# Kernel tuning notes

Hardware: AMD Instinct MI355X
Metric: run time of the kernel (lower is better)

The kernel has to match this reference:

```python
import jax, jax.numpy as jnp
import numpy as np

DEPTH = 6
HEADS = 8
DIM = 512
DH = DIM // HEADS          # 64
SEQ = 512
BATCH = 8
MEM = 4096                 # KNN memory slots per batch element (scaled from 64000)
TOPK = 32                  # num_retrieved_memories
KNN_LAYERS = (3, 4)        # memorizing_layers=(4,5), 1-indexed -> 0-indexed 3,4
FF = 4 * DIM


def setup_inputs() -> dict:
    key = jax.random.key(0)
    ks = jax.random.split(key, 18)
    s = 0.02
    return {
        "x":     jax.random.normal(ks[0], (BATCH, SEQ, DIM), jnp.float32),
        "Wq":    jax.random.normal(ks[1], (DEPTH, DIM, DIM), jnp.float32) * s,
        "Wk":    jax.random.normal(ks[2], (DEPTH, DIM, DIM), jnp.float32) * s,
        "Wv":    jax.random.normal(ks[3], (DEPTH, DIM, DIM), jnp.float32) * s,
        "Wo":    jax.random.normal(ks[4], (DEPTH, DIM, DIM), jnp.float32) * s,
        "ln1_s": jnp.ones((DEPTH, DIM), jnp.float32),
        "ln1_b": jnp.zeros((DEPTH, DIM), jnp.float32),
        "ln2_s": jnp.ones((DEPTH, DIM), jnp.float32),
        "ln2_b": jnp.zeros((DEPTH, DIM), jnp.float32),
        "W1":    jax.random.normal(ks[5], (DEPTH, DIM, FF), jnp.float32) * s,
        "W2":    jax.random.normal(ks[6], (DEPTH, FF, DIM), jnp.float32) * s,
        "lnf_s": jnp.ones((DIM,), jnp.float32),
        "lnf_b": jnp.zeros((DIM,), jnp.float32),
        # pre-populated KNN memory banks (keys/values in head dim), one per memorizing layer
        "mem_k": jax.random.normal(ks[7], (len(KNN_LAYERS), BATCH, MEM, DH), jnp.float32),
        "mem_v": jax.random.normal(ks[8], (len(KNN_LAYERS), BATCH, MEM, DH), jnp.float32),
    }


def _ln(x, s, b):
    m = x.mean(-1, keepdims=True)
    v = ((x - m) ** 2).mean(-1, keepdims=True)
    return (x - m) * jax.lax.rsqrt(v + 1e-5) * s + b


def _gather_mem(mem, idx):
    # mem: (b, M, d), idx: (b, h, n, K) -> (b, h, n, K, d)
    return jax.vmap(lambda m, i: m[i])(mem, idx)


def reference(x, Wq, Wk, Wv, Wo, ln1_s, ln1_b, ln2_s, ln2_b, W1, W2,
              lnf_s, lnf_b, mem_k, mem_v):
    b, n, d = x.shape
    scale = DH ** -0.5
    causal = jnp.tril(jnp.ones((n, n), dtype=bool))
    neg = jnp.float32(-1e9)
    mem_i = 0
    for l in range(DEPTH):
        h = _ln(x, ln1_s[l], ln1_b[l])
        q = (h @ Wq[l]).reshape(b, n, HEADS, DH)
        k = (h @ Wk[l]).reshape(b, n, HEADS, DH)
        v = (h @ Wv[l]).reshape(b, n, HEADS, DH)
        sim = jnp.einsum('bihd,bjhd->bhij', q, k) * scale
        sim = jnp.where(causal, sim, neg)
        if l in KNN_LAYERS:
            mk, mv = mem_k[mem_i], mem_v[mem_i]              # (b, M, dh)
            # KNN search: dense scoring + top-k retrieval
            sim_all = jnp.einsum('bihd,bmd->bhim', q, mk) * scale  # (b,h,n,M)
            top_sim, top_idx = jax.lax.top_k(sim_all, TOPK)        # (b,h,n,K)
            gv = _gather_mem(mv, top_idx)                          # (b,h,n,K,dh)
            # joint softmax over [retrieved memories, local causal]
            logits = jnp.concatenate([top_sim, sim], axis=-1)
            attn = jax.nn.softmax(logits, axis=-1)
            a_mem, a_loc = attn[..., :TOPK], attn[..., TOPK:]
            out = (jnp.einsum('bhik,bhikd->bhid', a_mem, gv)
                   + jnp.einsum('bhij,bjhd->bhid', a_loc, v))
            mem_i += 1
        else:
            attn = jax.nn.softmax(sim, axis=-1)
            out = jnp.einsum('bhij,bjhd->bhid', attn, v)
        out = out.transpose(0, 2, 1, 3).reshape(b, n, d) @ Wo[l]
        x = x + out
        h2 = _ln(x, ln2_s[l], ln2_b[l])
        x = x + jax.nn.gelu(h2 @ W1[l]) @ W2[l]
    return _ln(x, lnf_s, lnf_b)
```

## Files before the change

kernel.cpp:

```cpp
#include <hip/hip_runtime.h>
#include <math.h>

#define BB 8
#define NN 512
#define DD 512
#define HH 8
#define DHH 64
#define FFF 2048
#define MEMM 4096
#define TOPKK 32
#define DEPTHH 6
#define NT (BB*NN)

typedef __bf16 bf16x8 __attribute__((ext_vector_type(8)));
typedef __bf16 bf16x4 __attribute__((ext_vector_type(4)));
typedef float f32x4 __attribute__((ext_vector_type(4)));

template <int OBF16>
__global__ __launch_bounds__(256) void ln_kernel(const float* __restrict__ xin,
                                                 const float* __restrict__ g,
                                                 const float* __restrict__ bt,
                                                 void* __restrict__ outv) {
  __shared__ float red[4];
  int tok = blockIdx.x;
  const float* xr = xin + (size_t)tok * DD;
  int t = threadIdx.x;
  float v0 = xr[t], v1 = xr[t + 256];
  float s = v0 + v1;
#pragma unroll
  for (int m = 32; m; m >>= 1) s += __shfl_xor(s, m, 64);
  if ((t & 63) == 0) red[t >> 6] = s;
  __syncthreads();
  float mean = (red[0] + red[1] + red[2] + red[3]) * (1.0f / 512.0f);
  float d0 = v0 - mean, d1 = v1 - mean;
  float vv = d0 * d0 + d1 * d1;
#pragma unroll
  for (int m = 32; m; m >>= 1) vv += __shfl_xor(vv, m, 64);
  __syncthreads();
  if ((t & 63) == 0) red[t >> 6] = vv;
  __syncthreads();
  float var = (red[0] + red[1] + red[2] + red[3]) * (1.0f / 512.0f);
  float inv = rsqrtf(var + 1e-5f);
  float o0 = d0 * inv * g[t] + bt[t];
  float o1 = d1 * inv * g[t + 256] + bt[t + 256];
  if (OBF16) {
    __bf16* out = (__bf16*)outv;
    out[(size_t)tok * DD + t] = (__bf16)o0;
    out[(size_t)tok * DD + t + 256] = (__bf16)o1;
  } else {
    float* out = (float*)outv;
    out[(size_t)tok * DD + t] = o0;
    out[(size_t)tok * DD + t + 256] = o1;
  }
}

__device__ inline float gelu_f(float x) {
  float x3 = x * x * x;
  return 0.5f * x * (1.0f + tanhf(0.7978845608028654f * (x + 0.044715f * x3)));
}

__global__ __launch_bounds__(256) void transpose_bf16_kernel(const float* __restrict__ src,
                                                             __bf16* __restrict__ dst,
                                                             int K, int N) {
  __shared__ float tile[32][33];
  int n0 = blockIdx.x * 32, k0 = blockIdx.y * 32;
  int tx = threadIdx.x & 31, ty = threadIdx.x >> 5;
#pragma unroll
  for (int i = 0; i < 4; i++) {
    int r = ty + i * 8;
    tile[r][tx] = src[(size_t)(k0 + r) * N + n0 + tx];
  }
  __syncthreads();
#pragma unroll
  for (int i = 0; i < 4; i++) {
    int r = ty + i * 8;
    dst[(size_t)(n0 + r) * K + k0 + tx] = (__bf16)tile[tx][r];
  }
}

template <int EPI, int OBF16>
__global__ __launch_bounds__(256) void gemm_mfma(const __bf16* __restrict__ A,
                                                 const __bf16* __restrict__ Bt,
                                                 const float* __restrict__ R,
                                                 void* __restrict__ Cout,
                                                 int M, int N, int K) {
  __shared__ __bf16 Als[128 * 72];
  __shared__ __bf16 Bls[64 * 72];
  int t = threadIdx.x;
  int bn = blockIdx.x, bm = blockIdx.y;
  int lane = t & 63, wave = t >> 6;
  int wr = wave >> 1, wc = wave & 1;
  int m15 = lane & 15, q = lane >> 4;
  f32x4 acc[4][2] = {};
  for (int kt = 0; kt < K; kt += 64) {
    __syncthreads();
#pragma unroll
    for (int i = 0; i < 4; i++) {
      int c = t + i * 256;
      int row = c >> 3, pb = c & 7;
      *(uint4*)&Als[row * 72 + pb * 8] =
          *(const uint4*)(A + (size_t)(bm * 128 + row) * K + kt + pb * 8);
    }
#pragma unroll
    for (int i = 0; i < 2; i++) {
      int c = t + i * 256;
      int row = c >> 3, pb = c & 7;
      *(uint4*)&Bls[row * 72 + pb * 8] =
          *(const uint4*)(Bt + (size_t)(bn * 64 + row) * K + kt + pb * 8);
    }
    __syncthreads();
#pragma unroll
    for (int ks = 0; ks < 2; ks++) {
      bf16x8 af[4], bf[2];
#pragma unroll
      for (int mt = 0; mt < 4; mt++)
        af[mt] = *(const bf16x8*)&Als[(wr * 64 + mt * 16 + m15) * 72 + (ks * 4 + q) * 8];
#pragma unroll
      for (int nt = 0; nt < 2; nt++)
        bf[nt] = *(const bf16x8*)&Bls[(wc * 32 + nt * 16 + m15) * 72 + (ks * 4 + q) * 8];
#pragma unroll
      for (int mt = 0; mt < 4; mt++)
#pragma unroll
        for (int nt = 0; nt < 2; nt++)
          acc[mt][nt] = __builtin_amdgcn_mfma_f32_16x16x32_bf16(af[mt], bf[nt],
                                                                acc[mt][nt], 0, 0, 0);
    }
  }
#pragma unroll
  for (int mt = 0; mt < 4; mt++) {
#pragma unroll
    for (int nt = 0; nt < 2; nt++) {
      int gc = bn * 64 + wc * 32 + nt * 16 + m15;
#pragma unroll
      for (int r = 0; r < 4; r++) {
        int gr = bm * 128 + wr * 64 + mt * 16 + q * 4 + r;
        size_t off = (size_t)gr * N + gc;
        float v = acc[mt][nt][r];
        if (EPI == 1) v = gelu_f(v);
        if (EPI == 2) v += R[off];
        if (OBF16) ((__bf16*)Cout)[off] = (__bf16)v;
        else       ((float*)Cout)[off] = v;
      }
    }
  }
}

__global__ __launch_bounds__(256) void split_bf16_kernel(const float* __restrict__ src,
                                                         __bf16* __restrict__ hi,
                                                         __bf16* __restrict__ lo) {
  int i = blockIdx.x * 256 + threadIdx.x;
  float4 v = ((const float4*)src)[i];
  float xs[4] = {v.x, v.y, v.z, v.w};
  bf16x4 hv, lv;
#pragma unroll
  for (int e = 0; e < 4; e++) {
    __bf16 h = (__bf16)xs[e];
    hv[e] = h;
    lv[e] = (__bf16)(xs[e] - (float)h);
  }
  *(bf16x4*)&hi[(size_t)i * 4] = hv;
  *(bf16x4*)&lo[(size_t)i * 4] = lv;
}

__global__ __launch_bounds__(256) void vtrans_split_kernel(const float* __restrict__ v,
                                                           __bf16* __restrict__ vth,
                                                           __bf16* __restrict__ vtl) {
  __shared__ float tile[64 * 68];
  int tt = blockIdx.x, h = blockIdx.y, b = blockIdx.z;
  int t = threadIdx.x;
#pragma unroll
  for (int i = 0; i < 4; i++) {
    int lin = i * 256 + t, row = lin >> 4, c = (lin & 15) * 4;
    float4 x = *(const float4*)(v + ((size_t)(b * NN) + tt * 64 + row) * DD + h * DHH + c);
    *(float4*)&tile[row * 68 + c] = x;
  }
  __syncthreads();
  int d = t >> 2, tb = (t & 3) * 16;
  float xs[16];
#pragma unroll
  for (int j = 0; j < 16; j++) xs[j] = tile[(tb + j) * 68 + d];
  bf16x8 h0, h1, l0, l1;
#pragma unroll
  for (int j = 0; j < 8; j++) {
    __bf16 a = (__bf16)xs[j];
    h0[j] = a; l0[j] = (__bf16)(xs[j] - (float)a);
    __bf16 bmv = (__bf16)xs[8 + j];
    h1[j] = bmv; l1[j] = (__bf16)(xs[8 + j] - (float)bmv);
  }
  size_t ob = ((size_t)(b * HH + h) * 64 + d) * NN + tt * 64 + tb;
  *(bf16x8*)(vth + ob) = h0; *(bf16x8*)(vth + ob + 8) = h1;
  *(bf16x8*)(vtl + ob) = l0; *(bf16x8*)(vtl + ob + 8) = l1;
}

__global__ __launch_bounds__(256) void knn_score_mfma(const float* __restrict__ q,
                                                      const __bf16* __restrict__ khi,
                                                      const __bf16* __restrict__ klo,
                                                      float* __restrict__ S,
                                                      int bh0) {
  __shared__ __bf16 Kls[2][128 * 72];
  int it = blockIdx.x, bh = bh0 + blockIdx.y;
  int b = bh >> 3, h = bh & 7;
  int t = threadIdx.x;
  int lane = t & 63, w = t >> 6;
  int m15 = lane & 15, kg = lane >> 4;
  const float scale = 0.125f;

  bf16x8 aqh[2][2], aql[2][2];
#pragma unroll
  for (int rf = 0; rf < 2; rf++)
#pragma unroll
    for (int ks = 0; ks < 2; ks++) {
      const float* qp = q + ((size_t)(b * NN) + it * 32 + rf * 16 + m15) * DD +
                        h * DHH + ks * 32 + kg * 8;
      float4 x0 = *(const float4*)qp;
      float4 x1 = *(const float4*)(qp + 4);
      float xs[8] = {x0.x, x0.y, x0.z, x0.w, x1.x, x1.y, x1.z, x1.w};
#pragma unroll
      for (int e = 0; e < 8; e++) {
        __bf16 hv = (__bf16)xs[e];
        aqh[rf][ks][e] = hv;
        aql[rf][ks][e] = (__bf16)(xs[e] - (float)hv);
      }
    }

  const __bf16* khb = khi + (size_t)b * MEMM * DHH;
  const __bf16* klb = klo + (size_t)b * MEMM * DHH;
  size_t srow0 = (size_t)blockIdx.y * NN + it * 32;

  for (int mt = 0; mt < MEMM; mt += 128) {
    __syncthreads();
#pragma unroll
    for (int i = 0; i < 4; i++) {
      int lin = i * 256 + t;
      int row = lin >> 3, cb = (lin & 7) * 8;
      *(uint4*)&Kls[0][row * 72 + cb] = *(const uint4*)(khb + (size_t)(mt + row) * DHH + cb);
      *(uint4*)&Kls[1][row * 72 + cb] = *(const uint4*)(klb + (size_t)(mt + row) * DHH + cb);
    }
    __syncthreads();
    f32x4 acc[2][2] = {};
#pragma unroll
    for (int ks = 0; ks < 2; ks++) {
      bf16x8 bh2[2], bl2[2];
#pragma unroll
      for (int cf = 0; cf < 2; cf++) {
        int row = w * 32 + cf * 16 + m15;
        bh2[cf] = *(const bf16x8*)&Kls[0][row * 72 + ks * 32 + kg * 8];
        bl2[cf] = *(const bf16x8*)&Kls[1][row * 72 + ks * 32 + kg * 8];
      }
#pragma unroll
      for (int rf = 0; rf < 2; rf++)
#pragma unroll
        for (int cf = 0; cf < 2; cf++) {
          acc[rf][cf] = __builtin_amdgcn_mfma_f32_16x16x32_bf16(aqh[rf][ks], bh2[cf], acc[rf][cf], 0, 0, 0);
          acc[rf][cf] = __builtin_amdgcn_mfma_f32_16x16x32_bf16(aql[rf][ks], bh2[cf], acc[rf][cf], 0, 0, 0);
          acc[rf][cf] = __builtin_amdgcn_mfma_f32_16x16x32_bf16(aqh[rf][ks], bl2[cf], acc[rf][cf], 0, 0, 0);
        }
    }
#pragma unroll
    for (int rf = 0; rf < 2; rf++)
#pragma unroll
      for (int cf = 0; cf < 2; cf++) {
        int col = mt + w * 32 + cf * 16 + m15;
#pragma unroll
        for (int rr = 0; rr < 4; rr++)
          S[(srow0 + rf * 16 + kg * 4 + rr) * MEMM + col] = acc[rf][cf][rr] * scale;
      }
  }
}

__global__ __launch_bounds__(256, 4) void knn_select_kernel(const float* __restrict__ S,
                                                            float* __restrict__ topv,
                                                            int* __restrict__ topi,
                                                            int row_base) {
  int lane = threadIdx.x & 63;
  int row = blockIdx.x * 4 + (threadIdx.x >> 6);
  const float* srow = S + (size_t)row * MEMM;
  unsigned u[64];
#pragma unroll
  for (int i = 0; i < 64; i++) {
    union { float f; unsigned b; } cv;
    cv.f = srow[i * 64 + lane];
    unsigned b = cv.b;
    u[i] = (b & 0x80000000u) ? ~b : (b | 0x80000000u);
  }
  unsigned T = 0;
#pragma unroll 1
  for (int bit = 31; bit >= 0; --bit) {
    unsigned Tp = T | (1u << bit);
    int c = 0;
#pragma unroll
    for (int i = 0; i < 64; i++) c += (u[i] >= Tp) ? 1 : 0;
#pragma unroll
    for (int m = 32; m; m >>= 1) c += __shfl_xor(c, m, 64);
    if (c >= TOPKK) {
      T = Tp;
      if (c == TOPKK) break;
    }
  }
  unsigned long long below = (1ull << lane) - 1ull;
  float* tvrow = topv + (size_t)(row_base + row) * TOPKK;
  int* tirow = topi + (size_t)(row_base + row) * TOPKK;
  int g = 0;
#pragma unroll
  for (int i = 0; i < 64; i++) {
    bool f = u[i] > T;
    unsigned long long m = __ballot(f);
    if (f) {
      int pos = g + __popcll(m & below);
      union { unsigned b; float f2; } rv;
      rv.b = (u[i] & 0x80000000u) ? (u[i] & 0x7fffffffu) : ~u[i];
      tvrow[pos] = rv.f2;
      tirow[pos] = i * 64 + lane;
    }
    g += __popcll(m);
  }
#pragma unroll
  for (int i = 0; i < 64; i++) {
    if (g < TOPKK) {
      bool f = (u[i] == T);
      unsigned long long m = __ballot(f);
      if (f) {
        int pos = g + __popcll(m & below);
        if (pos < TOPKK) {
          union { unsigned b; float f2; } rv;
          rv.b = (T & 0x80000000u) ? (T & 0x7fffffffu) : ~T;
          tvrow[pos] = rv.f2;
          tirow[pos] = i * 64 + lane;
        }
      }
      g += __popcll(m);
    }
  }
}

__device__ __forceinline__ void insert32vi(float (&rtv)[32], int (&rti)[32],
                                           float sv, int idx, float& thr) {
  float mv = rtv[0], mv2 = INFINITY;
  int mi = 0;
#pragma unroll
  for (int k = 1; k < 32; k++) {
    float v = rtv[k];
    bool lt = v < mv;
    mv2 = lt ? mv : fminf(mv2, v);
    mv = lt ? v : mv;
    mi = lt ? k : mi;
  }
#pragma unroll
  for (int k = 0; k < 32; k++) {
    bool hit = (k == mi);
    rtv[k] = hit ? sv : rtv[k];
    rti[k] = hit ? idx : rti[k];
  }
  thr = fminf(mv2, sv);
}

__global__ __launch_bounds__(256) void knn_mfma_topk(const float* __restrict__ q,
                                                     const __bf16* __restrict__ khi,
                                                     const __bf16* __restrict__ klo,
                                                     float* __restrict__ topv,
                                                     int* __restrict__ topi) {
  __shared__ __bf16 Kls[2][128 * 72];
  __shared__ float scb[32][132];
  __shared__ unsigned short midx[32 * 260];
  __shared__ float rthr[8][32];
  int it = blockIdx.x, h = blockIdx.y, b = blockIdx.z;
  int t = threadIdx.x;
  int lane = t & 63, w = t >> 6;
  int m15 = lane & 15, kg = lane >> 4;
  const float scale = 0.125f;
  bf16x8 aqh[2][2], aql[2][2];
#pragma unroll
  for (int rf = 0; rf < 2; rf++)
#pragma unroll
    for (int ks = 0; ks < 2; ks++) {
      const float* qp = q + ((size_t)(b * NN) + it * 32 + rf * 16 + m15) * DD +
                        h * DHH + ks * 32 + kg * 8;
      float4 x0 = *(const float4*)qp;
      float4 x1 = *(const float4*)(qp + 4);
      float xs[8] = {x0.x, x0.y, x0.z, x0.w, x1.x, x1.y, x1.z, x1.w};
#pragma unroll
      for (int e = 0; e < 8; e++) {
        __bf16 hv = (__bf16)xs[e];
        aqh[rf][ks][e] = hv;
        aql[rf][ks][e] = (__bf16)(xs[e] - (float)hv);
      }
    }
  int r = t & 31, p = t >> 5;
  rthr[p][r] = -INFINITY;
  float rtv[32]; int rti[32];
#pragma unroll
  for (int k = 0; k < 32; k++) { rtv[k] = -INFINITY; rti[k] = 0; }
  float thr = -INFINITY;
  const __bf16* khb = khi + (size_t)b * MEMM * DHH;
  const __bf16* klb = klo + (size_t)b * MEMM * DHH;

  for (int mt = 0; mt < MEMM; mt += 128) {
    __syncthreads();
#pragma unroll
    for (int i = 0; i < 4; i++) {
      int lin = i * 256 + t;
      int row = lin >> 3, cb = (lin & 7) * 8;
      *(uint4*)&Kls[0][row * 72 + cb] = *(const uint4*)(khb + (size_t)(mt + row) * DHH + cb);
      *(uint4*)&Kls[1][row * 72 + cb] = *(const uint4*)(klb + (size_t)(mt + row) * DHH + cb);
    }
    __syncthreads();
    f32x4 acc[2][2] = {};
#pragma unroll
    for (int ks = 0; ks < 2; ks++) {
      bf16x8 bh2[2], bl2[2];
#pragma unroll
      for (int cf = 0; cf < 2; cf++) {
        int row = w * 32 + cf * 16 + m15;
        bh2[cf] = *(const bf16x8*)&Kls[0][row * 72 + ks * 32 + kg * 8];
        bl2[cf] = *(const bf16x8*)&Kls[1][row * 72 + ks * 32 + kg * 8];
      }
#pragma unroll
      for (int rf = 0; rf < 2; rf++)
#pragma unroll
        for (int cf = 0; cf < 2; cf++) {
          acc[rf][cf] = __builtin_amdgcn_mfma_f32_16x16x32_bf16(aqh[rf][ks], bh2[cf], acc[rf][cf], 0, 0, 0);
          acc[rf][cf] = __builtin_amdgcn_mfma_f32_16x16x32_bf16(aql[rf][ks], bh2[cf], acc[rf][cf], 0, 0, 0);
          acc[rf][cf] = __builtin_amdgcn_mfma_f32_16x16x32_bf16(aqh[rf][ks], bl2[cf], acc[rf][cf], 0, 0, 0);
        }
    }
#pragma unroll
    for (int rf = 0; rf < 2; rf++)
#pragma unroll
      for (int cf = 0; cf < 2; cf++) {
        int col = w * 32 + cf * 16 + m15;
#pragma unroll
        for (int rr = 0; rr < 4; rr++)
          scb[rf * 16 + kg * 4 + rr][col] = acc[rf][cf][rr] * scale;
      }
    __syncthreads();
    {
      float B2 = rthr[0][r];
#pragma unroll
      for (int j = 1; j < 8; j++) B2 = fmaxf(B2, rthr[j][r]);
      const float* srow = &scb[r][16 * p];
#pragma unroll 1
      for (int c = 0; c < 16; c++) {
        int cc = (c + r) & 15;
        float sv = srow[cc];
        if (sv > fmaxf(thr, B2))
          insert32vi(rtv, rti, sv, mt + 16 * p + cc, thr);
      }
      rthr[p][r] = thr;
    }
  }
  __syncthreads();
  float* mvals = (float*)&Kls[0][0];
#pragma unroll
  for (int k = 0; k < 32; k++) {
    int cc = (k + r) & 31;
    mvals[(size_t)260 * r + 32 * p + cc] = rtv[k];
    midx[(size_t)260 * r + 32 * p + cc] = (unsigned short)rti[k];
  }
  __syncthreads();
  if (t < 32) {
#pragma unroll 1
    for (int c = 0; c < 224; c++) {
      int cc = c + r; if (cc >= 224) cc -= 224;
      float sv = mvals[(size_t)260 * r + 32 + cc];
      if (sv > thr)
        insert32vi(rtv, rti, sv, (int)midx[(size_t)260 * r + 32 + cc], thr);
    }
    size_t rowg = ((size_t)b * HH + h) * NN + it * 32 + r;
#pragma unroll
    for (int k = 0; k < 32; k++) {
      topv[rowg * TOPKK + k] = rtv[k];
      topi[rowg * TOPKK + k] = rti[k];
    }
  }
}

__global__ __launch_bounds__(256) void attn_mfma_kernel(
    const float* __restrict__ q, const float* __restrict__ kf,
    const __bf16* __restrict__ vth, const __bf16* __restrict__ vtl,
    __bf16* __restrict__ ao, const float* __restrict__ topv,
    const int* __restrict__ topi, const float* __restrict__ mem_v, int knn) {
  __shared__ __align__(16) __bf16 smem[27648];
  __bf16* Kh = smem;
  __bf16* Kl = smem + 4608;
  __bf16* Vh = smem + 9216;
  __bf16* Vl = smem + 13824;
  __bf16* Pw = smem + 18432;

  int bi = blockIdx.x, h = blockIdx.y, b = blockIdx.z;
  int t = threadIdx.x, lane = t & 63, w = t >> 6;
  int q15 = lane & 15, g = lane >> 4;
  const float scale = 0.125f;

  bf16x8 qh[2], ql[2];
  {
    const float* qp = q + ((size_t)(b * NN) + bi * 64 + w * 16 + q15) * DD + h * DHH;
#pragma unroll
    for (int ks = 0; ks < 2; ks++) {
      float4 x0 = *(const float4*)(qp + ks * 32 + g * 8);
      float4 x1 = *(const float4*)(qp + ks * 32 + g * 8 + 4);
      float xs[8] = {x0.x, x0.y, x0.z, x0.w, x1.x, x1.y, x1.z, x1.w};
#pragma unroll
      for (int e = 0; e < 8; e++) {
        __bf16 hv = (__bf16)xs[e];
        qh[ks][e] = hv;
        ql[ks][e] = (__bf16)(xs[e] - (float)hv);
      }
    }
  }
  float m_run = -INFINITY, l_run = 0.f;
  f32x4 opv[4] = {};
  int ntiles = bi + 1;
  for (int jt = 0; jt < ntiles; jt++) {
    __syncthreads();
#pragma unroll
    for (int i = 0; i < 4; i++) {
      int lin = i * 256 + t, row = lin >> 4, c = (lin & 15) * 4;
      float4 kx = *(const float4*)(kf + ((size_t)(b * NN) + jt * 64 + row) * DD + h * DHH + c);
      float ks4[4] = {kx.x, kx.y, kx.z, kx.w};
      bf16x4 hv, lv;
#pragma unroll
      for (int e = 0; e < 4; e++) {
        __bf16 a = (__bf16)ks4[e];
        hv[e] = a; lv[e] = (__bf16)(ks4[e] - (float)a);
      }
      *(bf16x4*)&Kh[row * 72 + c] = hv;
      *(bf16x4*)&Kl[row * 72 + c] = lv;
    }
#pragma unroll
    for (int i = 0; i < 2; i++) {
      int lin = i * 256 + t, d = lin >> 3, tb = (lin & 7) * 8;
      size_t go = ((size_t)(b * HH + h) * 64 + d) * NN + jt * 64 + tb;
      *(uint4*)&Vh[d * 72 + tb] = *(const uint4*)(vth + go);
      *(uint4*)&Vl[d * 72 + tb] = *(const uint4*)(vtl + go);
    }
    __syncthreads();
    int smax = (jt == bi) ? w : 3;
    float sc16[16];
    float tmax = -INFINITY;
#pragma unroll
    for (int s = 0; s < 4; s++) {
      if (s <= smax) {
        f32x4 accs = {};
#pragma unroll
        for (int ks = 0; ks < 2; ks++) {
          bf16x8 ah = *(const bf16x8*)&Kh[(s * 16 + q15) * 72 + ks * 32 + g * 8];
          bf16x8 al = *(const bf16x8*)&Kl[(s * 16 + q15) * 72 + ks * 32 + g * 8];
          accs = __builtin_amdgcn_mfma_f32_16x16x32_bf16(ah, qh[ks], accs, 0, 0, 0);
          accs = __builtin_amdgcn_mfma_f32_16x16x32_bf16(al, qh[ks], accs, 0, 0, 0);
          accs = __builtin_amdgcn_mfma_f32_16x16x32_bf16(ah, ql[ks], accs, 0, 0, 0);
        }
#pragma unroll
        for (int r = 0; r < 4; r++) {
          float sv = accs[r] * scale;
          if (jt == bi) {
            int kvg = jt * 64 + s * 16 + g * 4 + r;
            int qg = bi * 64 + w * 16 + q15;
            if (kvg > qg) sv = -INFINITY;
          }
          sc16[s * 4 + r] = sv;
          tmax = fmaxf(tmax, sv);
        }
      } else {
#pragma unroll
        for (int r = 0; r < 4; r++) sc16[s * 4 + r] = -INFINITY;
      }
    }
    tmax = fmaxf(tmax, __shfl_xor(tmax, 16, 64));
    tmax = fmaxf(tmax, __shfl_xor(tmax, 32, 64));
    float m_new = fmaxf(m_run, tmax);
    float psum = 0.f;
    __bf16 ph[16], pl[16];
#pragma unroll
    for (int i = 0; i < 16; i++) {
      float p = __expf(sc16[i] - m_new);
      psum += p;
      __bf16 hp = (__bf16)p;
      ph[i] = hp; pl[i] = (__bf16)(p - (float)hp);
    }
    psum += __shfl_xor(psum, 16, 64);
    psum += __shfl_xor(psum, 32, 64);
    float alpha = __expf(m_run - m_new);
    l_run = l_run * alpha + psum;
    m_run = m_new;
    __bf16* Ph = Pw + (w * 2 + 0) * 1152;
    __bf16* Pl = Pw + (w * 2 + 1) * 1152;
#pragma unroll
    for (int s = 0; s < 4; s++) {
      bf16x4 hv, lv;
#pragma unroll
      for (int r = 0; r < 4; r++) { hv[r] = ph[s * 4 + r]; lv[r] = pl[s * 4 + r]; }
      *(bf16x4*)&Ph[q15 * 72 + s * 16 + g * 4] = hv;
      *(bf16x4*)&Pl[q15 * 72 + s * 16 + g * 4] = lv;
    }
    __builtin_amdgcn_wave_barrier();
    float a0 = __shfl(alpha, g * 4 + 0, 64);
    float a1 = __shfl(alpha, g * 4 + 1, 64);
    float a2 = __shfl(alpha, g * 4 + 2, 64);
    float a3 = __shfl(alpha, g * 4 + 3, 64);
#pragma unroll
    for (int dsub = 0; dsub < 4; dsub++) {
      opv[dsub][0] *= a0; opv[dsub][1] *= a1;
      opv[dsub][2] *= a2; opv[dsub][3] *= a3;
    }
#pragma unroll
    for (int ks2 = 0; ks2 < 2; ks2++) {
      bf16x8 pah = *(const bf16x8*)&Ph[q15 * 72 + ks2 * 32 + g * 8];
      bf16x8 pal = *(const bf16x8*)&Pl[q15 * 72 + ks2 * 32 + g * 8];
#pragma unroll
      for (int dsub = 0; dsub < 4; dsub++) {
        bf16x8 vbh = *(const bf16x8*)&Vh[(dsub * 16 + q15) * 72 + ks2 * 32 + g * 8];
        bf16x8 vbl = *(const bf16x8*)&Vl[(dsub * 16 + q15) * 72 + ks2 * 32 + g * 8];
        opv[dsub] = __builtin_amdgcn_mfma_f32_16x16x32_bf16(pah, vbh, opv[dsub], 0, 0, 0);
        opv[dsub] = __builtin_amdgcn_mfma_f32_16x16x32_bf16(pal, vbh, opv[dsub], 0, 0, 0);
        opv[dsub] = __builtin_amdgcn_mfma_f32_16x16x32_bf16(pah, vbl, opv[dsub], 0, 0, 0);
      }
    }
  }
  __syncthreads();
  float* scf  = (float*)smem;
  float* marr = (float*)(smem + 8704);
  float* larr = marr + 64;
  float* aarr = marr + 128;
  float* sc2  = (float*)(smem + 9216);
  int*   pidx = (int*)(smem + 13824);
#pragma unroll
  for (int dsub = 0; dsub < 4; dsub++)
#pragma unroll
    for (int r = 0; r < 4; r++)
      scf[(w * 16 + g * 4 + r) * 68 + dsub * 16 + q15] = opv[dsub][r];
  if (g == 0) { marr[w * 16 + q15] = m_run; larr[w * 16 + q15] = l_run; }
  __syncthreads();
  int r_ = t & 63, w4 = t >> 6;
  float acc16[16];
  if (knn) {
    size_t rowbase = ((size_t)b * HH + h) * NN + bi * 64;
    for (int rr = w * 16; rr < w * 16 + 16; rr++) {
      float s = (lane < TOPKK) ? topv[(rowbase + rr) * TOPKK + lane] : -INFINITY;
      float m_old = marr[rr];
      float tm = s;
#pragma unroll
      for (int m = 32; m; m >>= 1) tm = fmaxf(tm, __shfl_xor(tm, m, 64));
      float m_new = fmaxf(m_old, tm);
      float p = __expf(s - m_new);
      float ts = p;
#pragma unroll
      for (int m = 32; m; m >>= 1) ts += __shfl_xor(ts, m, 64);
      float alpha = __expf(m_old - m_new);
      if (lane < TOPKK) {
        sc2[rr * 33 + lane] = p;
        pidx[rr * 32 + lane] = topi[(rowbase + rr) * TOPKK + lane];
      }
      if (lane == 0) {
        marr[rr] = m_new; larr[rr] = larr[rr] * alpha + ts; aarr[rr] = alpha;
      }
    }
    __syncthreads();
    float al = aarr[r_];
#pragma unroll
    for (int dd = 0; dd < 16; dd++) acc16[dd] = scf[r_ * 68 + w4 * 16 + dd] * al;
    const float* mvb = mem_v + (size_t)b * MEMM * DHH;
#pragma unroll 1
    for (int kk = 0; kk < TOPKK; kk++) {
      float p = sc2[r_ * 33 + kk];
      const float* mrow = mvb + (size_t)pidx[r_ * 32 + kk] * DHH + w4 * 16;
#pragma unroll
      for (int dd = 0; dd < 16; dd += 4) {
        float4 m4 = *(const float4*)(mrow + dd);
        acc16[dd] += p * m4.x; acc16[dd + 1] += p * m4.y;
        acc16[dd + 2] += p * m4.z; acc16[dd + 3] += p * m4.w;
      }
    }
  } else {
#pragma unroll
    for (int dd = 0; dd < 16; dd++) acc16[dd] = scf[r_ * 68 + w4 * 16 + dd];
  }
  float linv = 1.f / larr[r_];
  bf16x8 o0, o1;
#pragma unroll
  for (int j = 0; j < 8; j++) {
    o0[j] = (__bf16)(acc16[j] * linv);
    o1[j] = (__bf16)(acc16[8 + j] * linv);
  }
  __bf16* aop = ao + ((size_t)(b * NN) + bi * 64 + r_) * DD + h * DHH + w4 * 16;
  *(bf16x8*)aop = o0;
  *(bf16x8*)(aop + 8) = o1;
}

extern "C" void kernel_launch(void* const* d_in, const int* in_sizes, int n_in,
                              void* d_out, int out_size, void* d_ws, size_t ws_size,
                              hipStream_t stream) {
  const float* x_in  = (const float*)d_in[0];
  const float* Wq    = (const float*)d_in[1];
  const float* Wk    = (const float*)d_in[2];
  const float* Wv    = (const float*)d_in[3];
  const float* Wo    = (const float*)d_in[4];
  const float* ln1_s = (const float*)d_in[5];
  const float* ln1_b = (const float*)d_in[6];
  const float* ln2_s = (const float*)d_in[7];
  const float* ln2_b = (const float*)d_in[8];
  const float* W1    = (const float*)d_in[9];
  const float* W2    = (const float*)d_in[10];
  const float* lnf_s = (const float*)d_in[11];
  const float* lnf_b = (const float*)d_in[12];
  const float* mem_k = (const float*)d_in[13];
  const float* mem_v = (const float*)d_in[14];

  float* ws  = (float*)d_ws;
  float*  xb    = ws;
  float*  qb    = ws + 2097152;
  float*  kb    = ws + 4194304;
  float*  vb    = ws + 6291456;
  __bf16* hb16  = (__bf16*)(ws + 8388608);
  __bf16* ao16  = (__bf16*)(ws + 9437184);
  __bf16* wqT   = (__bf16*)(ws + 10485760);
  __bf16* wkT   = (__bf16*)(ws + 10616832);
  __bf16* wvT   = (__bf16*)(ws + 10747904);
  __bf16* woT   = (__bf16*)(ws + 10878976);
  __bf16* w1T   = (__bf16*)(ws + 11010048);
  __bf16* w2T   = (__bf16*)(ws + 11534336);
  float*  tvb   = ws + 12058624;
  int*    tib   = (int*)(ws + 13107200);
  __bf16* ffb16 = (__bf16*)(ws + 2097152);
  __bf16* khi16 = (__bf16*)(ws + 8388608);
  __bf16* klo16 = (__bf16*)(ws + 9437184);

  const size_t base_floats = 14155776;
  const size_t slice_floats = (size_t)NN * MEMM;
  const size_t ws_floats = ws_size / sizeof(float);
  int nbh = 0;
  for (int c = 64; c >= 1; c >>= 1) {
    if (base_floats + (size_t)c * slice_floats <= ws_floats) { nbh = c; break; }
  }
  float* Sb = ws + base_floats;
  __bf16* vth = (__bf16*)(ws + base_floats);
  __bf16* vtl = (__bf16*)(ws + base_floats + 1048576);

  dim3 blk(256);
  const size_t DD2 = (size_t)DD * DD;
  for (int l = 0; l < DEPTHH; l++) {
    const float* xcur = (l == 0) ? x_in : xb;
    transpose_bf16_kernel<<<dim3(16, 16), blk, 0, stream>>>(Wq + l * DD2, wqT, DD, DD);
    transpose_bf16_kernel<<<dim3(16, 16), blk, 0, stream>>>(Wk + l * DD2, wkT, DD, DD);
    transpose_bf16_kernel<<<dim3(16, 16), blk, 0, stream>>>(Wv + l * DD2, wvT, DD, DD);
    transpose_bf16_kernel<<<dim3(16, 16), blk, 0, stream>>>(Wo + l * DD2, woT, DD, DD);
    transpose_bf16_kernel<<<dim3(64, 16), blk, 0, stream>>>(W1 + (size_t)l * DD * FFF, w1T, DD, FFF);
    transpose_bf16_kernel<<<dim3(16, 64), blk, 0, stream>>>(W2 + (size_t)l * FFF * DD, w2T, FFF, DD);

    ln_kernel<1><<<NT, blk, 0, stream>>>(xcur, ln1_s + l * DD, ln1_b + l * DD, hb16);
    gemm_mfma<0, 0><<<dim3(8, 32), blk, 0, stream>>>(hb16, wqT, nullptr, qb, NT, DD, DD);
    gemm_mfma<0, 0><<<dim3(8, 32), blk, 0, stream>>>(hb16, wkT, nullptr, kb, NT, DD, DD);
    gemm_mfma<0, 0><<<dim3(8, 32), blk, 0, stream>>>(hb16, wvT, nullptr, vb, NT, DD, DD);
    int mi = (l == 3) ? 0 : ((l == 4) ? 1 : -1);
    if (mi >= 0) {
      const float* mk = mem_k + (size_t)mi * BB * MEMM * DHH;
      split_bf16_kernel<<<dim3(BB * MEMM * DHH / 1024), blk, 0, stream>>>(mk, khi16, klo16);
      if (nbh > 0) {
        for (int bh0 = 0; bh0 < BB * HH; bh0 += nbh) {
          knn_score_mfma<<<dim3(16, nbh), blk, 0, stream>>>(qb, khi16, klo16, Sb, bh0);
          knn_select_kernel<<<dim3(nbh * NN / 4), blk, 0, stream>>>(Sb, tvb, tib, bh0 * NN);
        }
      } else {
        knn_mfma_topk<<<dim3(16, 8, 8), blk, 0, stream>>>(qb, khi16, klo16, tvb, tib);
      }
    }
    vtrans_split_kernel<<<dim3(8, 8, 8), blk, 0, stream>>>(vb, vth, vtl);
    attn_mfma_kernel<<<dim3(8, 8, 8), blk, 0, stream>>>(
        qb, kb, vth, vtl, ao16, tvb, tib,
        mem_v + (size_t)(mi < 0 ? 0 : mi) * BB * MEMM * DHH, mi >= 0 ? 1 : 0);
    gemm_mfma<2, 0><<<dim3(8, 32), blk, 0, stream>>>(ao16, woT, xcur, xb, NT, DD, DD);
    ln_kernel<1><<<NT, blk, 0, stream>>>(xb, ln2_s + l * DD, ln2_b + l * DD, hb16);
    gemm_mfma<1, 1><<<dim3(32, 32), blk, 0, stream>>>(hb16, w1T, nullptr, ffb16, NT, FFF, DD);
    gemm_mfma<2, 0><<<dim3(8, 32), blk, 0, stream>>>(ffb16, w2T, xb, xb, NT, DD, FFF);
  }
  ln_kernel<0><<<NT, blk, 0, stream>>>(xb, lnf_s, lnf_b, (float*)d_out);
}
```

Before: 2.040 ms.

## Fuse QKV projections into one GEMM and enlarge GEMM tiles with direct LDS loads

Lays the transposed Wq, Wk and Wv contiguously so one GEMM produces a fused 1536-wide QKV buffer. Downstream KNN, V-transpose and attention kernels are re-indexed to read Q, K and V from it at a 1536 stride. The GEMM tile grows from 128x64 to 128x128, and loads now go global-to-LDS via global_load_lds without padding. This cuts launches and raises arithmetic intensity, but the unpadded LDS layout may cause bank conflicts, and the larger tile means fewer blocks for the 512-wide GEMMs.

```diff
diff --git a/kernel.cpp b/kernel.cpp
--- a/kernel.cpp
+++ b/kernel.cpp
@@ -11,6 +11,7 @@
 #define TOPKK 32
 #define DEPTHH 6
 #define NT (BB*NN)
+#define QKVS 1536
 
 typedef __bf16 bf16x8 __attribute__((ext_vector_type(8)));
 typedef __bf16 bf16x4 __attribute__((ext_vector_type(4)));
@@ -78,59 +79,59 @@
   }
 }
 
+__device__ __forceinline__ void gload16(const __bf16* g, __bf16* lds) {
+  __builtin_amdgcn_global_load_lds(
+      (const __attribute__((address_space(1))) void*)g,
+      (__attribute__((address_space(3))) void*)lds, 16, 0, 0);
+}
+
 template <int EPI, int OBF16>
-__global__ __launch_bounds__(256) void gemm_mfma(const __bf16* __restrict__ A,
-                                                 const __bf16* __restrict__ Bt,
-                                                 const float* __restrict__ R,
-                                                 void* __restrict__ Cout,
-                                                 int M, int N, int K) {
-  __shared__ __bf16 Als[128 * 72];
-  __shared__ __bf16 Bls[64 * 72];
+__global__ __launch_bounds__(256) void gemm_mfma128(const __bf16* __restrict__ A,
+                                                    const __bf16* __restrict__ Bt,
+                                                    const float* __restrict__ R,
+                                                    void* __restrict__ Cout,
+                                                    int M, int N, int K) {
+  __shared__ __align__(16) __bf16 Als[128 * 64];
+  __shared__ __align__(16) __bf16 Bls[128 * 64];
   int t = threadIdx.x;
   int bn = blockIdx.x, bm = blockIdx.y;
-  int lane = t & 63, wave = t >> 6;
-  int wr = wave >> 1, wc = wave & 1;
+  int lane = t & 63, w = t >> 6;
+  int wr = w >> 1, wc = w & 1;
   int m15 = lane & 15, q = lane >> 4;
-  f32x4 acc[4][2] = {};
+  f32x4 acc[4][4] = {};
   for (int kt = 0; kt < K; kt += 64) {
     __syncthreads();
 #pragma unroll
     for (int i = 0; i < 4; i++) {
-      int c = t + i * 256;
-      int row = c >> 3, pb = c & 7;
-      *(uint4*)&Als[row * 72 + pb * 8] =
-          *(const uint4*)(A + (size_t)(bm * 128 + row) * K + kt + pb * 8);
-    }
-#pragma unroll
-    for (int i = 0; i < 2; i++) {
-      int c = t + i * 256;
-      int row = c >> 3, pb = c & 7;
-      *(uint4*)&Bls[row * 72 + pb * 8] =
-          *(const uint4*)(Bt + (size_t)(bn * 64 + row) * K + kt + pb * 8);
+      int rg = w * 32 + i * 8;
+      int row = rg + (lane >> 3);
+      int lcol = (lane & 7) * 8;
+      gload16(A + (size_t)(bm * 128 + row) * K + kt + lcol, &Als[rg * 64]);
+      gload16(Bt + (size_t)(bn * 128 + row) * K + kt + lcol, &Bls[rg * 64]);
     }
     __syncthreads();
 #pragma unroll
     for (int ks = 0; ks < 2; ks++) {
-      bf16x8 af[4], bf[2];
+      bf16x8 af[4], bfr[4];
 #pragma unroll
       for (int mt = 0; mt < 4; mt++)
-        af[mt] = *(const bf16x8*)&Als[(wr * 64 + mt * 16 + m15) * 72 + (ks * 4 + q) * 8];
-#pragma unroll
-      for (int nt = 0; nt < 2; nt++)
-        bf[nt] = *(const bf16x8*)&Bls[(wc * 32 + nt * 16 + m15) * 72 + (ks * 4 + q) * 8];
+        af[mt] = *(const bf16x8*)&Als[(wr * 64 + mt * 16 + m15) * 64 + (ks * 4 + q) * 8];
+#pragma unroll
+      for (int nt = 0; nt < 4; nt++)
+        bfr[nt] = *(const bf16x8*)&Bls[(wc * 64 + nt * 16 + m15) * 64 + (ks * 4 + q) * 8];
 #pragma unroll
       for (int mt = 0; mt < 4; mt++)
 #pragma unroll
-        for (int nt = 0; nt < 2; nt++)
-          acc[mt][nt] = __builtin_amdgcn_mfma_f32_16x16x32_bf16(af[mt], bf[nt],
+        for (int nt = 0; nt < 4; nt++)
+          acc[mt][nt] = __builtin_amdgcn_mfma_f32_16x16x32_bf16(af[mt], bfr[nt],
                                                                 acc[mt][nt], 0, 0, 0);
     }
   }
 #pragma unroll
   for (int mt = 0; mt < 4; mt++) {
 #pragma unroll
-    for (int nt = 0; nt < 2; nt++) {
-      int gc = bn * 64 + wc * 32 + nt * 16 + m15;
+    for (int nt = 0; nt < 4; nt++) {
+      int gc = bn * 128 + wc * 64 + nt * 16 + m15;
 #pragma unroll
       for (int r = 0; r < 4; r++) {
         int gr = bm * 128 + wr * 64 + mt * 16 + q * 4 + r;
@@ -162,7 +163,7 @@
   *(bf16x4*)&lo[(size_t)i * 4] = lv;
 }
 
-__global__ __launch_bounds__(256) void vtrans_split_kernel(const float* __restrict__ v,
+__global__ __launch_bounds__(256) void vtrans_split_kernel(const float* __restrict__ qkv,
                                                            __bf16* __restrict__ vth,
                                                            __bf16* __restrict__ vtl) {
   __shared__ float tile[64 * 68];
@@ -171,7 +172,7 @@
 #pragma unroll
   for (int i = 0; i < 4; i++) {
     int lin = i * 256 + t, row = lin >> 4, c = (lin & 15) * 4;
-    float4 x = *(const float4*)(v + ((size_t)(b * NN) + tt * 64 + row) * DD + h * DHH + c);
+    float4 x = *(const float4*)(qkv + ((size_t)(b * NN) + tt * 64 + row) * QKVS + 1024 + h * DHH + c);
     *(float4*)&tile[row * 68 + c] = x;
   }
   __syncthreads();
@@ -210,7 +211,7 @@
   for (int rf = 0; rf < 2; rf++)
 #pragma unroll
     for (int ks = 0; ks < 2; ks++) {
-      const float* qp = q + ((size_t)(b * NN) + it * 32 + rf * 16 + m15) * DD +
+      const float* qp = q + ((size_t)(b * NN) + it * 32 + rf * 16 + m15) * QKVS +
                         h * DHH + ks * 32 + kg * 8;
       float4 x0 = *(const float4*)qp;
       float4 x1 = *(const float4*)(qp + 4);
@@ -373,7 +374,7 @@
   for (int rf = 0; rf < 2; rf++)
 #pragma unroll
     for (int ks = 0; ks < 2; ks++) {
-      const float* qp = q + ((size_t)(b * NN) + it * 32 + rf * 16 + m15) * DD +
+      const float* qp = q + ((size_t)(b * NN) + it * 32 + rf * 16 + m15) * QKVS +
                         h * DHH + ks * 32 + kg * 8;
       float4 x0 = *(const float4*)qp;
       float4 x1 = *(const float4*)(qp + 4);
@@ -475,7 +476,7 @@
 }
 
 __global__ __launch_bounds__(256) void attn_mfma_kernel(
-    const float* __restrict__ q, const float* __restrict__ kf,
+    const float* __restrict__ qkv,
     const __bf16* __restrict__ vth, const __bf16* __restrict__ vtl,
     __bf16* __restrict__ ao, const float* __restrict__ topv,
     const int* __restrict__ topi, const float* __restrict__ mem_v, int knn) {
@@ -493,7 +494,7 @@
 
   bf16x8 qh[2], ql[2];
   {
-    const float* qp = q + ((size_t)(b * NN) + bi * 64 + w * 16 + q15) * DD + h * DHH;
+    const float* qp = qkv + ((size_t)(b * NN) + bi * 64 + w * 16 + q15) * QKVS + h * DHH;
 #pragma unroll
     for (int ks = 0; ks < 2; ks++) {
       float4 x0 = *(const float4*)(qp + ks * 32 + g * 8);
@@ -515,7 +516,7 @@
 #pragma unroll
     for (int i = 0; i < 4; i++) {
       int lin = i * 256 + t, row = lin >> 4, c = (lin & 15) * 4;
-      float4 kx = *(const float4*)(kf + ((size_t)(b * NN) + jt * 64 + row) * DD + h * DHH + c);
+      float4 kx = *(const float4*)(qkv + ((size_t)(b * NN) + jt * 64 + row) * QKVS + 512 + h * DHH + c);
       float ks4[4] = {kx.x, kx.y, kx.z, kx.w};
       bf16x4 hv, lv;
 #pragma unroll
@@ -707,20 +708,18 @@
 
   float* ws  = (float*)d_ws;
   float*  xb    = ws;
-  float*  qb    = ws + 2097152;
-  float*  kb    = ws + 4194304;
-  float*  vb    = ws + 6291456;
+  float*  qkvb  = ws + 2097152;
   __bf16* hb16  = (__bf16*)(ws + 8388608);
   __bf16* ao16  = (__bf16*)(ws + 9437184);
   __bf16* wqT   = (__bf16*)(ws + 10485760);
-  __bf16* wkT   = (__bf16*)(ws + 10616832);
-  __bf16* wvT   = (__bf16*)(ws + 10747904);
   __bf16* woT   = (__bf16*)(ws + 10878976);
   __bf16* w1T   = (__bf16*)(ws + 11010048);
   __bf16* w2T   = (__bf16*)(ws + 11534336);
   float*  tvb   = ws + 12058624;
   int*    tib   = (int*)(ws + 13107200);
   __bf16* ffb16 = (__bf16*)(ws + 2097152);
+  __bf16* wkT   = wqT + 262144;
+  __bf16* wvT   = wqT + 524288;
   __bf16* khi16 = (__bf16*)(ws + 8388608);
   __bf16* klo16 = (__bf16*)(ws + 9437184);
 
@@ -747,30 +746,28 @@
     transpose_bf16_kernel<<<dim3(16, 64), blk, 0, stream>>>(W2 + (size_t)l * FFF * DD, w2T, FFF, DD);
 
     ln_kernel<1><<<NT, blk, 0, stream>>>(xcur, ln1_s + l * DD, ln1_b + l * DD, hb16);
-    gemm_mfma<0, 0><<<dim3(8, 32), blk, 0, stream>>>(hb16, wqT, nullptr, qb, NT, DD, DD);
-    gemm_mfma<0, 0><<<dim3(8, 32), blk, 0, stream>>>(hb16, wkT, nullptr, kb, NT, DD, DD);
-    gemm_mfma<0, 0><<<dim3(8, 32), blk, 0, stream>>>(hb16, wvT, nullptr, vb, NT, DD, DD);
+    gemm_mfma128<0, 0><<<dim3(12, 32), blk, 0, stream>>>(hb16, wqT, nullptr, qkvb, NT, QKVS, DD);
     int mi = (l == 3) ? 0 : ((l == 4) ? 1 : -1);
     if (mi >= 0) {
       const float* mk = mem_k + (size_t)mi * BB * MEMM * DHH;
       split_bf16_kernel<<<dim3(BB * MEMM * DHH / 1024), blk, 0, stream>>>(mk, khi16, klo16);
       if (nbh > 0) {
         for (int bh0 = 0; bh0 < BB * HH; bh0 += nbh) {
-          knn_score_mfma<<<dim3(16, nbh), blk, 0, stream>>>(qb, khi16, klo16, Sb, bh0);
+          knn_score_mfma<<<dim3(16, nbh), blk, 0, stream>>>(qkvb, khi16, klo16, Sb, bh0);
           knn_select_kernel<<<dim3(nbh * NN / 4), blk, 0, stream>>>(Sb, tvb, tib, bh0 * NN);
         }
       } else {
-        knn_mfma_topk<<<dim3(16, 8, 8), blk, 0, stream>>>(qb, khi16, klo16, tvb, tib);
-      }
-    }
-    vtrans_split_kernel<<<dim3(8, 8, 8), blk, 0, stream>>>(vb, vth, vtl);
+        knn_mfma_topk<<<dim3(16, 8, 8), blk, 0, stream>>>(qkvb, khi16, klo16, tvb, tib);
+      }
+    }
+    vtrans_split_kernel<<<dim3(8, 8, 8), blk, 0, stream>>>(qkvb, vth, vtl);
     attn_mfma_kernel<<<dim3(8, 8, 8), blk, 0, stream>>>(
-        qb, kb, vth, vtl, ao16, tvb, tib,
+        qkvb, vth, vtl, ao16, tvb, tib,
         mem_v + (size_t)(mi < 0 ? 0 : mi) * BB * MEMM * DHH, mi >= 0 ? 1 : 0);
-    gemm_mfma<2, 0><<<dim3(8, 32), blk, 0, stream>>>(ao16, woT, xcur, xb, NT, DD, DD);
+    gemm_mfma128<2, 0><<<dim3(4, 32), blk, 0, stream>>>(ao16, woT, xcur, xb, NT, DD, DD);
     ln_kernel<1><<<NT, blk, 0, stream>>>(xb, ln2_s + l * DD, ln2_b + l * DD, hb16);
-    gemm_mfma<1, 1><<<dim3(32, 32), blk, 0, stream>>>(hb16, w1T, nullptr, ffb16, NT, FFF, DD);
-    gemm_mfma<2, 0><<<dim3(8, 32), blk, 0, stream>>>(ffb16, w2T, xb, xb, NT, DD, FFF);
+    gemm_mfma128<1, 1><<<dim3(16, 32), blk, 0, stream>>>(hb16, w1T, nullptr, ffb16, NT, FFF, DD);
+    gemm_mfma128<2, 0><<<dim3(4, 32), blk, 0, stream>>>(ffb16, w2T, xb, xb, NT, DD, FFF);
   }
   ln_kernel<0><<<NT, blk, 0, stream>>>(xb, lnf_s, lnf_b, (float*)d_out);
 }
```

Result: no change. 2.070 ms (+1.5%).
